# Kernel tuning notes

Measured on AMD Instinct MI355X. Metric: run time of the kernel, lower is better.

The kernel has to match this reference:

```python
import jax, jax.numpy as jnp
import numpy as np

N = 4096
K = 8


def setup_inputs() -> dict:
    key = jax.random.key(0)
    kA, kb, ka, kZ, kC = jax.random.split(key, 5)
    A = (jax.random.uniform(kA, (N, N)) < 0.01).astype(jnp.float32)
    beta = jax.random.normal(kb, (N,), dtype=jnp.float32)
    a = jax.random.normal(ka, (1,), dtype=jnp.float32)
    Z = jax.random.normal(kZ, (K, N), dtype=jnp.float32)
    C = jax.random.normal(kC, (N, K), dtype=jnp.float32)
    return {"A": A, "beta": beta, "a": a, "Z": Z, "C": C}


def reference(A, beta, a, Z, C):
    # beta_ij = beta_i + beta_j  -> [N, N]
    beta2 = beta[:, None] + beta[None, :]
    Zs = jax.nn.softmax(Z, axis=0)          # [K, N], softmax over archetypes
    Cs = jax.nn.softmax(C, axis=0)          # [N, K], softmax over nodes
    # M = (Zs @ Cs @ Zs).T -> [N, K] latent positions
    M = (Zs @ (Cs @ Zs)).T
    # Pairwise euclidean distance with the original's +1e-6 shift inside the square.
    diff = M[:, None, :] - M[None, :, :] + 1e-6   # [N, N, K]
    z_dist = jnp.sqrt(jnp.sum(diff * diff, axis=-1))  # [N, N]
    theta = beta2 - a[0] * z_dist
    sp = jax.nn.softplus(theta)
    # Zero the diagonal (theta - diag(diagonal(theta)) zeroes diag entries).
    d = jnp.arange(N)
    theta_off = theta.at[d, d].set(0.0)
    sp_off = sp.at[d, d].set(0.0)
    LL = jnp.sum(theta_off * A) - jnp.sum(sp_off)
    return LL
```

## Files before the change

### kernel.cpp

```cpp
#include <hip/hip_runtime.h>

#define N 4096
#define K 8
#define NPB 16
#define S2_ROWS 4
#define S2_BLOCKS (N / S2_ROWS)
#define S1_IT 32
#define S1_JT 1024
#define S1_BLOCKS ((N / S1_IT) * (N / S1_JT))
#define HCAP 1024

__device__ __forceinline__ float fast_exp2(float x) { return __builtin_amdgcn_exp2f(x); }
__device__ __forceinline__ float fast_log2(float x) { return __builtin_amdgcn_logf(x); }
__device__ __forceinline__ float fast_sqrt(float x) { return __builtin_amdgcn_sqrtf(x); }

__global__ __launch_bounds__(256) void prep_stats(
    const float* __restrict__ Z, const float* __restrict__ C,
    float* __restrict__ ZsT, float* __restrict__ Upart, float* __restrict__ out)
{
    const int t = threadIdx.x;
    const int n = blockIdx.x * 256 + t;
    const float L2E = 1.44269504f;

    __shared__ float zsL[256 * K];
    __shared__ float eL[256 * K];
    __shared__ float red[4][64];

    if (blockIdx.x == 0 && t == 0) out[0] = 0.f;

    float z[K];
#pragma unroll
    for (int k = 0; k < K; ++k) z[k] = Z[k * N + n];
    float zmax = z[0];
#pragma unroll
    for (int k = 1; k < K; ++k) zmax = fmaxf(zmax, z[k]);
    float zs[K];
    float zsum = 0.f;
#pragma unroll
    for (int k = 0; k < K; ++k) { zs[k] = fast_exp2((z[k] - zmax) * L2E); zsum += zs[k]; }
    const float inv = 1.f / zsum;
#pragma unroll
    for (int k = 0; k < K; ++k) zs[k] *= inv;

    float4* zst_p = (float4*)(ZsT + (size_t)n * K);
    zst_p[0] = make_float4(zs[0], zs[1], zs[2], zs[3]);
    zst_p[1] = make_float4(zs[4], zs[5], zs[6], zs[7]);

    const float4* c_p = (const float4*)(C + (size_t)n * K);
    const float4 c0 = c_p[0], c1 = c_p[1];
    float e[K];
    e[0] = fast_exp2(c0.x * L2E); e[1] = fast_exp2(c0.y * L2E);
    e[2] = fast_exp2(c0.z * L2E); e[3] = fast_exp2(c0.w * L2E);
    e[4] = fast_exp2(c1.x * L2E); e[5] = fast_exp2(c1.y * L2E);
    e[6] = fast_exp2(c1.z * L2E); e[7] = fast_exp2(c1.w * L2E);

#pragma unroll
    for (int k = 0; k < K; ++k) { zsL[t * K + k] = zs[k]; eL[t * K + k] = e[k]; }
    __syncthreads();

    const int cell = t & 63, q = t >> 6;
    const int a = cell >> 3, b = cell & 7;
    float s = 0.f;
    const int n0 = q * 64;
#pragma unroll 4
    for (int nn = 0; nn < 64; ++nn)
        s = fmaf(zsL[(n0 + nn) * K + a], eL[(n0 + nn) * K + b], s);
    red[q][cell] = s;
    __syncthreads();
    if (t < 64)
        Upart[blockIdx.x * 64 + t] = red[0][t] + red[1][t] + red[2][t] + red[3][t];
}

__global__ __launch_bounds__(256) void prep_M(
    const float* __restrict__ ZsT, const float* __restrict__ Upart,
    const float* __restrict__ A, const float* __restrict__ beta,
    const float* __restrict__ a_ptr, float* __restrict__ RowConst,
    float* __restrict__ ColConst, float* __restrict__ out)
{
    const int t = threadIdx.x;
    const int n = blockIdx.x * 256 + t;
    const float L2E = 1.44269504f;
    const float LN2 = 0.69314718f;

    __shared__ float UL[64];
    __shared__ float SinvL[8];
    if (t < 64) {
        float s = 0.f;
#pragma unroll
        for (int blk = 0; blk < NPB; ++blk) s += Upart[blk * 64 + t];
        UL[t] = s;
    }
    __syncthreads();
    if (t < 8) {
        float s = 0.f;
#pragma unroll
        for (int a = 0; a < 8; ++a) s += UL[a * 8 + t];
        SinvL[t] = 1.f / s;
    }
    __syncthreads();

    const float4* zst_p = (const float4*)(ZsT + (size_t)n * K);
    const float4 z0 = zst_p[0], z1 = zst_p[1];
    float w[K];
    w[0] = z0.x * SinvL[0]; w[1] = z0.y * SinvL[1]; w[2] = z0.z * SinvL[2]; w[3] = z0.w * SinvL[3];
    w[4] = z1.x * SinvL[4]; w[5] = z1.y * SinvL[5]; w[6] = z1.z * SinvL[6]; w[7] = z1.w * SinvL[7];
    float m[K];
#pragma unroll
    for (int k = 0; k < K; ++k) {
        float acc = 0.f;
#pragma unroll
        for (int kk = 0; kk < K; ++kk) acc = fmaf(UL[k * K + kk], w[kk], acc);
        m[k] = acc;
    }

    float v[K];
    float s2r = 0.f, s2c = 0.f;
#pragma unroll
    for (int k = 0; k < K; ++k) {
        v[k] = m[k] + 1e-6f;
        s2r = fmaf(v[k], v[k], s2r);
        s2c = fmaf(m[k], m[k], s2c);
    }
    const float bL2E = beta[n] * L2E;
    float4* rr_p = (float4*)(RowConst + (size_t)n * 12);
    rr_p[0] = make_float4(-2.f * v[0], -2.f * v[1], -2.f * v[2], -2.f * v[3]);
    rr_p[1] = make_float4(-2.f * v[4], -2.f * v[5], -2.f * v[6], -2.f * v[7]);
    rr_p[2] = make_float4(s2r, bL2E, 0.f, 0.f);
    float4* cc_p = (float4*)(ColConst + (size_t)n * 12);
    cc_p[0] = make_float4(m[0], m[1], m[2], m[3]);
    cc_p[1] = make_float4(m[4], m[5], m[6], m[7]);
    cc_p[2] = make_float4(s2c, bL2E, 0.f, 0.f);

    const float av = A[(size_t)n * N + n];
    const float theta = fmaf(-a_ptr[0], 2.8284271247e-6f, 2.f * beta[n]);
    const float ex = fast_exp2(theta * L2E);
    const float sp = LN2 * fast_log2(1.f + ex);
    float d = fmaf(theta, av, -sp);

    for (int off = 32; off > 0; off >>= 1) d += __shfl_down(d, off, 64);
    __shared__ float wsum[4];
    const int lane = t & 63, wid = t >> 6;
    if (lane == 0) wsum[wid] = d;
    __syncthreads();
    if (t == 0) atomicAdd(out, -(wsum[0] + wsum[1] + wsum[2] + wsum[3]));
}

__global__ __launch_bounds__(256, 4) void pair_fused(
    const float* __restrict__ A, const float* __restrict__ RowConst,
    const float* __restrict__ ColConst, const float* __restrict__ a_ptr,
    float* __restrict__ out)
{
    const int t = threadIdx.x;
    const int lane = t & 63, w = t >> 6;
    const int bid = blockIdx.x;
    const float LN2 = 0.69314718f;
    const float naL2E = -a_ptr[0] * 1.44269504f;

    __shared__ __align__(16) float sL[S1_IT * 12];
    __shared__ int hcnt;
    __shared__ int hbuf[HCAP];
    __shared__ float wsum[4];

    float acc = 0.f;

    if (bid < S2_BLOCKS) {
        const int i0 = bid * S2_ROWS;
        if (t == 0) hcnt = 0;
        if (t < S2_ROWS) {
            const float4* rp = (const float4*)(RowConst + (size_t)(i0 + t) * 12);
            float4* dp = (float4*)&sL[t * 12];
            dp[0] = rp[0]; dp[1] = rp[1]; dp[2] = rp[2];
        }
        __syncthreads();

        const float4* A4 = (const float4*)A + (size_t)i0 * (N / 4);
        float acc_t = 0.f;

#pragma unroll
        for (int b = 0; b < 2; ++b) {
            float4 v[8];
#pragma unroll
            for (int s = 0; s < 8; ++s) {
                const int r = b * 2 + (s >> 2);
                const int k = s & 3;
                v[s] = A4[r * (N / 4) + k * 256 + t];
            }
            float sm[8];
            float tot = 0.f;
#pragma unroll
            for (int s = 0; s < 8; ++s) {
                sm[s] = (v[s].x + v[s].y) + (v[s].z + v[s].w);
                tot += sm[s];
            }
            if (tot != 0.f) {
#pragma unroll
                for (int s = 0; s < 8; ++s) {
                    if (sm[s] != 0.f) {
                        const int r = b * 2 + (s >> 2);
                        const int jb = ((s & 3) * 256 + t) * 4;
                        const float ae[4] = { v[s].x, v[s].y, v[s].z, v[s].w };
#pragma unroll
                        for (int e = 0; e < 4; ++e) {
                            if (ae[e] != 0.f) {
                                const int idx = atomicAdd(&hcnt, 1);
                                if (idx < HCAP) {
                                    hbuf[idx] = (r << 12) | (jb + e);
                                } else {
                                    const float* cp = ColConst + (size_t)(jb + e) * 12;
                                    const float4 m0 = *(const float4*)cp;
                                    const float4 m1 = *(const float4*)(cp + 4);
                                    const float2 cb = *(const float2*)(cp + 8);
                                    const float4 ti0 = *(const float4*)&sL[r * 12];
                                    const float4 ti1 = *(const float4*)&sL[r * 12 + 4];
                                    float ss = sL[r * 12 + 8] + cb.x;
                                    ss = fmaf(ti0.x, m0.x, ss); ss = fmaf(ti0.y, m0.y, ss);
                                    ss = fmaf(ti0.z, m0.z, ss); ss = fmaf(ti0.w, m0.w, ss);
                                    ss = fmaf(ti1.x, m1.x, ss); ss = fmaf(ti1.y, m1.y, ss);
                                    ss = fmaf(ti1.z, m1.z, ss); ss = fmaf(ti1.w, m1.w, ss);
                                    ss = fmaxf(ss, 0.f);
                                    acc_t = fmaf(naL2E, fast_sqrt(ss), acc_t + sL[r * 12 + 9] + cb.y);
                                }
                            }
                        }
                    }
                }
            }
        }
        __syncthreads();

        const int cnt = min(hcnt, HCAP);
        for (int h = t; h < cnt; h += 256) {
            const int ecode = hbuf[h];
            const int r = ecode >> 12;
            const int j = ecode & 4095;
            const float* cp = ColConst + (size_t)j * 12;
            const float4 m0 = *(const float4*)cp;
            const float4 m1 = *(const float4*)(cp + 4);
            const float2 cb = *(const float2*)(cp + 8);
            const float4 ti0 = *(const float4*)&sL[r * 12];
            const float4 ti1 = *(const float4*)&sL[r * 12 + 4];
            float ss = sL[r * 12 + 8] + cb.x;
            ss = fmaf(ti0.x, m0.x, ss); ss = fmaf(ti0.y, m0.y, ss);
            ss = fmaf(ti0.z, m0.z, ss); ss = fmaf(ti0.w, m0.w, ss);
            ss = fmaf(ti1.x, m1.x, ss); ss = fmaf(ti1.y, m1.y, ss);
            ss = fmaf(ti1.z, m1.z, ss); ss = fmaf(ti1.w, m1.w, ss);
            ss = fmaxf(ss, 0.f);
            const float dist = fast_sqrt(ss);
            acc_t += fmaf(naL2E, dist, sL[r * 12 + 9] + cb.y);
        }
        acc = LN2 * acc_t;
    } else {
        const int s = bid - S2_BLOCKS;
        const int it = s & (N / S1_IT - 1);
        const int jt = s >> 7;
        const int i0 = it * S1_IT;
        const int j0 = jt * S1_JT + 4 * t;

        if (t < S1_IT) {
            const float4* rp = (const float4*)(RowConst + (size_t)(i0 + t) * 12);
            float4* dp = (float4*)&sL[t * 12];
            dp[0] = rp[0]; dp[1] = rp[1]; dp[2] = rp[2];
        }
        __syncthreads();

        float4 mj0[4], mj1[4];
        float nj[4], bj[4];
#pragma unroll
        for (int c = 0; c < 4; ++c) {
            const float* cp = ColConst + (size_t)(j0 + c) * 12;
            mj0[c] = *(const float4*)cp;
            mj1[c] = *(const float4*)(cp + 4);
            const float2 cb = *(const float2*)(cp + 8);
            nj[c] = cb.x; bj[c] = cb.y;
        }

        float acc_l = 0.f;
        for (int r = 0; r < S1_IT; ++r) {
            const float4 ti0 = *(const float4*)&sL[r * 12];
            const float4 ti1 = *(const float4*)&sL[r * 12 + 4];
            const float ci = sL[r * 12 + 8];
            const float bi = sL[r * 12 + 9];
#pragma unroll
            for (int c = 0; c < 4; ++c) {
                float ss = ci + nj[c];
                ss = fmaf(ti0.x, mj0[c].x, ss); ss = fmaf(ti0.y, mj0[c].y, ss);
                ss = fmaf(ti0.z, mj0[c].z, ss); ss = fmaf(ti0.w, mj0[c].w, ss);
                ss = fmaf(ti1.x, mj1[c].x, ss); ss = fmaf(ti1.y, mj1[c].y, ss);
                ss = fmaf(ti1.z, mj1[c].z, ss); ss = fmaf(ti1.w, mj1[c].w, ss);
                ss = fmaxf(ss, 0.f);
                const float dist = fast_sqrt(ss);
                const float t2 = fmaf(naL2E, dist, bi + bj[c]);
                acc_l += fast_log2(1.f + fast_exp2(t2));
            }
        }
        acc = -LN2 * acc_l;
    }

    for (int off = 32; off > 0; off >>= 1) acc += __shfl_down(acc, off, 64);
    if (lane == 0) wsum[w] = acc;
    __syncthreads();
    if (t == 0) atomicAdd(out, wsum[0] + wsum[1] + wsum[2] + wsum[3]);
}

extern "C" void kernel_launch(void* const* d_in, const int* in_sizes, int n_in,
                              void* d_out, int out_size, void* d_ws, size_t ws_size,
                              hipStream_t stream)
{
    const float* A    = (const float*)d_in[0];
    const float* beta = (const float*)d_in[1];
    const float* a    = (const float*)d_in[2];
    const float* Z    = (const float*)d_in[3];
    const float* C    = (const float*)d_in[4];
    float* out = (float*)d_out;

    float* ws       = (float*)d_ws;
    float* ZsT      = ws;
    float* Upart    = ws + (size_t)N * K;
    float* RowConst = ws + (size_t)N * K + NPB * 64;
    float* ColConst = RowConst + (size_t)N * 12;

    prep_stats<<<NPB, 256, 0, stream>>>(Z, C, ZsT, Upart, out);
    prep_M<<<NPB, 256, 0, stream>>>(ZsT, Upart, A, beta, a, RowConst, ColConst, out);

    pair_fused<<<S2_BLOCKS + S1_BLOCKS, 256, 0, stream>>>(A, RowConst, ColConst, a, out);
}
```

Before: 122.4 us.

## Stream adjacency rows into LDS with async double-buffered loads and interleave block types

The sparse-A scan blocks now copy adjacency rows into a double-buffered LDS tile using global_load_lds, prefetching the next 1024-column chunk while the current one is scanned. Blocks are also interleaved so every third block does the dense pairwise softplus work and the other two scan A, which mixes memory-bound and compute-bound work on each CU. The change adds 32KB of LDS per block, which may limit occupancy under launch_bounds(256,4). It also puts a barrier at each of the four chunks, and there is no explicit wait for the async LDS loads to complete.

```diff
diff --git a/kernel.cpp b/kernel.cpp
--- a/kernel.cpp
+++ b/kernel.cpp
@@ -4,15 +4,24 @@
 #define K 8
 #define NPB 16
 #define S2_ROWS 4
-#define S2_BLOCKS (N / S2_ROWS)
+#define S2_BLOCKS 1024
+#define CCH 1024
+#define NCH (N / CCH)
 #define S1_IT 32
 #define S1_JT 1024
-#define S1_BLOCKS ((N / S1_IT) * (N / S1_JT))
-#define HCAP 1024
+#define S1_BLOCKS 512
+#define TOT_BLOCKS (S2_BLOCKS + S1_BLOCKS)
+#define HCAP 1536
 
 __device__ __forceinline__ float fast_exp2(float x) { return __builtin_amdgcn_exp2f(x); }
 __device__ __forceinline__ float fast_log2(float x) { return __builtin_amdgcn_logf(x); }
 __device__ __forceinline__ float fast_sqrt(float x) { return __builtin_amdgcn_sqrtf(x); }
+
+__device__ __forceinline__ void load_lds_16B(const float* g, float* l) {
+    __builtin_amdgcn_global_load_lds((const __attribute__((address_space(1))) void*)g,
+                                     (__attribute__((address_space(3))) void*)l,
+                                     16, 0, 0);
+}
 
 __global__ __launch_bounds__(256) void prep_stats(
     const float* __restrict__ Z, const float* __restrict__ C,
@@ -152,79 +161,80 @@
 {
     const int t = threadIdx.x;
     const int lane = t & 63, w = t >> 6;
-    const int bid = blockIdx.x;
     const float LN2 = 0.69314718f;
     const float naL2E = -a_ptr[0] * 1.44269504f;
 
+    __shared__ __align__(16) float Abuf[2][S2_ROWS][CCH];
     __shared__ __align__(16) float sL[S1_IT * 12];
+    __shared__ int hbuf[HCAP];
     __shared__ int hcnt;
-    __shared__ int hbuf[HCAP];
     __shared__ float wsum[4];
 
+    const int bid = blockIdx.x;
+    const int m3 = bid % 3;
     float acc = 0.f;
 
-    if (bid < S2_BLOCKS) {
-        const int i0 = bid * S2_ROWS;
+    if (m3 != 2) {
+        const int s2id = (bid / 3) * 2 + m3;
+        const int i0 = s2id * S2_ROWS;
         if (t == 0) hcnt = 0;
         if (t < S2_ROWS) {
             const float4* rp = (const float4*)(RowConst + (size_t)(i0 + t) * 12);
             float4* dp = (float4*)&sL[t * 12];
             dp[0] = rp[0]; dp[1] = rp[1]; dp[2] = rp[2];
         }
-        __syncthreads();
-
-        const float4* A4 = (const float4*)A + (size_t)i0 * (N / 4);
+
+        {
+            const float* g = A + (size_t)(i0 + w) * N + lane * 4;
+#pragma unroll
+            for (int s = 0; s < 4; ++s)
+                load_lds_16B(g + s * 256, &Abuf[0][w][s * 256]);
+        }
+
         float acc_t = 0.f;
-
-#pragma unroll
-        for (int b = 0; b < 2; ++b) {
-            float4 v[8];
-#pragma unroll
-            for (int s = 0; s < 8; ++s) {
-                const int r = b * 2 + (s >> 2);
-                const int k = s & 3;
-                v[s] = A4[r * (N / 4) + k * 256 + t];
+        int buf = 0;
+        for (int ch = 0; ch < NCH; ++ch) {
+            __syncthreads();
+            if (ch + 1 < NCH) {
+                const float* g = A + (size_t)(i0 + w) * N + (ch + 1) * CCH + lane * 4;
+#pragma unroll
+                for (int s = 0; s < 4; ++s)
+                    load_lds_16B(g + s * 256, &Abuf[buf ^ 1][w][s * 256]);
             }
-            float sm[8];
-            float tot = 0.f;
-#pragma unroll
-            for (int s = 0; s < 8; ++s) {
-                sm[s] = (v[s].x + v[s].y) + (v[s].z + v[s].w);
-                tot += sm[s];
-            }
-            if (tot != 0.f) {
-#pragma unroll
-                for (int s = 0; s < 8; ++s) {
-                    if (sm[s] != 0.f) {
-                        const int r = b * 2 + (s >> 2);
-                        const int jb = ((s & 3) * 256 + t) * 4;
-                        const float ae[4] = { v[s].x, v[s].y, v[s].z, v[s].w };
-#pragma unroll
-                        for (int e = 0; e < 4; ++e) {
-                            if (ae[e] != 0.f) {
-                                const int idx = atomicAdd(&hcnt, 1);
-                                if (idx < HCAP) {
-                                    hbuf[idx] = (r << 12) | (jb + e);
-                                } else {
-                                    const float* cp = ColConst + (size_t)(jb + e) * 12;
-                                    const float4 m0 = *(const float4*)cp;
-                                    const float4 m1 = *(const float4*)(cp + 4);
-                                    const float2 cb = *(const float2*)(cp + 8);
-                                    const float4 ti0 = *(const float4*)&sL[r * 12];
-                                    const float4 ti1 = *(const float4*)&sL[r * 12 + 4];
-                                    float ss = sL[r * 12 + 8] + cb.x;
-                                    ss = fmaf(ti0.x, m0.x, ss); ss = fmaf(ti0.y, m0.y, ss);
-                                    ss = fmaf(ti0.z, m0.z, ss); ss = fmaf(ti0.w, m0.w, ss);
-                                    ss = fmaf(ti1.x, m1.x, ss); ss = fmaf(ti1.y, m1.y, ss);
-                                    ss = fmaf(ti1.z, m1.z, ss); ss = fmaf(ti1.w, m1.w, ss);
-                                    ss = fmaxf(ss, 0.f);
-                                    acc_t = fmaf(naL2E, fast_sqrt(ss), acc_t + sL[r * 12 + 9] + cb.y);
-                                }
+            const int jc = ch * CCH + t * 4;
+#pragma unroll
+            for (int r = 0; r < S2_ROWS; ++r) {
+                const float4 v = *(const float4*)(&Abuf[buf][r][t * 4]);
+                const float sm = (v.x + v.y) + (v.z + v.w);
+                if (sm != 0.f) {
+                    const float ae[4] = { v.x, v.y, v.z, v.w };
+#pragma unroll
+                    for (int e = 0; e < 4; ++e) {
+                        if (ae[e] != 0.f) {
+                            const int idx = atomicAdd(&hcnt, 1);
+                            if (idx < HCAP) {
+                                hbuf[idx] = (r << 12) | (jc + e);
+                            } else {
+                                const float* cp = ColConst + (size_t)(jc + e) * 12;
+                                const float4 m0 = *(const float4*)cp;
+                                const float4 m1 = *(const float4*)(cp + 4);
+                                const float2 cb = *(const float2*)(cp + 8);
+                                const float4 ti0 = *(const float4*)&sL[r * 12];
+                                const float4 ti1 = *(const float4*)&sL[r * 12 + 4];
+                                float ss = sL[r * 12 + 8] + cb.x;
+                                ss = fmaf(ti0.x, m0.x, ss); ss = fmaf(ti0.y, m0.y, ss);
+                                ss = fmaf(ti0.z, m0.z, ss); ss = fmaf(ti0.w, m0.w, ss);
+                                ss = fmaf(ti1.x, m1.x, ss); ss = fmaf(ti1.y, m1.y, ss);
+                                ss = fmaf(ti1.z, m1.z, ss); ss = fmaf(ti1.w, m1.w, ss);
+                                ss = fmaxf(ss, 0.f);
+                                acc_t += fmaf(naL2E, fast_sqrt(ss),
+                                              sL[r * 12 + 9] + cb.y);
                             }
                         }
                     }
                 }
             }
+            buf ^= 1;
         }
         __syncthreads();
 
@@ -245,14 +255,13 @@
             ss = fmaf(ti1.x, m1.x, ss); ss = fmaf(ti1.y, m1.y, ss);
             ss = fmaf(ti1.z, m1.z, ss); ss = fmaf(ti1.w, m1.w, ss);
             ss = fmaxf(ss, 0.f);
-            const float dist = fast_sqrt(ss);
-            acc_t += fmaf(naL2E, dist, sL[r * 12 + 9] + cb.y);
+            acc_t += fmaf(naL2E, fast_sqrt(ss), sL[r * 12 + 9] + cb.y);
         }
         acc = LN2 * acc_t;
     } else {
-        const int s = bid - S2_BLOCKS;
-        const int it = s & (N / S1_IT - 1);
-        const int jt = s >> 7;
+        const int s1id = bid / 3;
+        const int it = s1id & (N / S1_IT - 1);
+        const int jt = s1id >> 7;
         const int i0 = it * S1_IT;
         const int j0 = jt * S1_JT + 4 * t;
 
@@ -322,5 +331,5 @@
     prep_stats<<<NPB, 256, 0, stream>>>(Z, C, ZsT, Upart, out);
     prep_M<<<NPB, 256, 0, stream>>>(ZsT, Upart, A, beta, a, RowConst, ColConst, out);
 
-    pair_fused<<<S2_BLOCKS + S1_BLOCKS, 256, 0, stream>>>(A, RowConst, ColConst, a, out);
-}
+    pair_fused<<<TOT_BLOCKS, 256, 0, stream>>>(A, RowConst, ColConst, a, out);
+}
```

Result: slower. 126.5 us (+3.4%).
